# Kernel optimization log

Measured on AMD Instinct MI355X. Metric: run time of the kernel, lower is better.

## Reference

```python
import jax, jax.numpy as jnp
import numpy as np

D_MODEL = 1024
N_HEADS = 16
D_K = D_MODEL // N_HEADS
SEQ = 2048
BATCH = 2
THETA = 10000.0


def _rope(x, token_positions):
    # x: [b, h, s, dk]; token_positions: [s] int
    k = jnp.arange(0, D_K, 2, dtype=jnp.float32)
    freqs = 1.0 / (THETA ** (k / D_K))                    # [dk/2]
    angles = token_positions.astype(jnp.float32)[:, None] * freqs[None, :]  # [s, dk/2]
    cos = jnp.cos(angles)
    sin = jnp.sin(angles)
    x1 = x[..., 0::2]
    x2 = x[..., 1::2]
    r1 = x1 * cos - x2 * sin
    r2 = x1 * sin + x2 * cos
    out = jnp.stack([r1, r2], axis=-1)                    # [b,h,s,dk/2,2]
    return out.reshape(x.shape)


def setup_inputs() -> dict:
    key = jax.random.key(0)
    ks = jax.random.split(key, 5)
    sigma = np.sqrt(2.0 / (D_MODEL + D_MODEL))
    x = jax.random.normal(ks[0], (BATCH, SEQ, D_MODEL), dtype=jnp.float32)
    Wq = jax.random.truncated_normal(ks[1], -3.0, 3.0, (D_MODEL, D_MODEL), dtype=jnp.float32) * sigma
    Wk = jax.random.truncated_normal(ks[2], -3.0, 3.0, (D_MODEL, D_MODEL), dtype=jnp.float32) * sigma
    Wv = jax.random.truncated_normal(ks[3], -3.0, 3.0, (D_MODEL, D_MODEL), dtype=jnp.float32) * sigma
    Wo = jax.random.truncated_normal(ks[4], -3.0, 3.0, (D_MODEL, D_MODEL), dtype=jnp.float32) * sigma
    token_positions = jnp.arange(SEQ, dtype=jnp.int64)
    return {"x": x, "Wq": Wq, "Wk": Wk, "Wv": Wv, "Wo": Wo, "token_positions": token_positions}


def reference(x, Wq, Wk, Wv, Wo, token_positions):
    b, s, d = x.shape
    # projections: Linear stores weight [out,in], applies x @ W.T
    Q = x @ Wq.T
    K = x @ Wk.T
    V = x @ Wv.T
    # [b, s, h*dk] -> [b, h, s, dk]
    def split_heads(t):
        return t.reshape(b, s, N_HEADS, D_K).transpose(0, 2, 1, 3)
    Q, K, V = split_heads(Q), split_heads(K), split_heads(V)
    Q = _rope(Q, token_positions)
    K = _rope(K, token_positions)
    scale = 1.0 / np.sqrt(D_K).astype(np.float32)
    scores = jnp.einsum('bhqd,bhkd->bhqk', Q, K) * scale   # [b,h,s,s]
    causal = jnp.tril(jnp.ones((s, s), dtype=bool))
    scores = jnp.where(causal, scores, -jnp.inf)
    attn = jax.nn.softmax(scores, axis=-1)
    out = jnp.einsum('bhqk,bhkd->bhqd', attn, V)           # [b,h,s,dk]
    out = out.transpose(0, 2, 1, 3).reshape(b, s, d)
    return out @ Wo.T
```

## Files before the change

kernel.cpp:

```cpp
#include <hip/hip_runtime.h>
#include <hip/hip_bf16.h>
#include <stdint.h>

#define SEQL   2048
#define NBATCH 2
#define BSZ    4096
#define DMODEL 1024
#define NH     16
#define DK     64
#define NBH    32
#define NCHUNK_TOT 40

typedef __attribute__((ext_vector_type(8)))  short short8;
typedef __attribute__((ext_vector_type(4)))  short shortx4;
typedef __attribute__((ext_vector_type(4)))  float f32x4;
typedef __attribute__((ext_vector_type(16))) float f32x16;
typedef __attribute__((ext_vector_type(4)))  unsigned uint4v;
union PU { uint4v u; short8 s; };

__device__ __forceinline__ short f2b(float f) {
  unsigned u = __float_as_uint(f);
  u = (u + 0x7FFF + ((u >> 16) & 1)) >> 16;
  return (short)u;
}
__device__ __forceinline__ float b2f(short s) {
  return __uint_as_float(((unsigned)(unsigned short)s) << 16);
}
__device__ __forceinline__ unsigned cvtpk(float lo, float hi) {
  unsigned r;
  asm("v_cvt_pk_bf16_f32 %0, %1, %2" : "=v"(r) : "v"(lo), "v"(hi));
  return r;
}

__device__ __forceinline__ void g2l16(const void* g, void* l) {
  __builtin_amdgcn_global_load_lds(
      (__attribute__((address_space(1))) void*)(uintptr_t)g,
      (__attribute__((address_space(3))) void*)l, 16, 0, 0);
}

__device__ __forceinline__ f32x4 mfma16(short8 a, short8 b, f32x4 c) {
  return __builtin_amdgcn_mfma_f32_16x16x32_bf16(a, b, c, 0, 0, 0);
}
__device__ __forceinline__ f32x16 mfma32(short8 a, short8 b, f32x16 c) {
  return __builtin_amdgcn_mfma_f32_32x32x16_bf16(a, b, c, 0, 0, 0);
}

__global__ void cvt_all(const float* __restrict__ x,  const float* __restrict__ wq,
                        const float* __restrict__ wk, const float* __restrict__ wv,
                        const float* __restrict__ wo, short* __restrict__ xb,
                        short* __restrict__ wqkv, short* __restrict__ wob) {
  long idx = ((long)blockIdx.x * 256 + threadIdx.x) * 4;
  const float* s; short* d; long off;
  if (idx < 4194304L)      { s = x;  d = xb;             off = idx; }
  else if (idx < 5242880L) { s = wq; d = wqkv;           off = idx - 4194304L; }
  else if (idx < 6291456L) { s = wk; d = wqkv + 1048576; off = idx - 5242880L; }
  else if (idx < 7340032L) { s = wv; d = wqkv + 2097152; off = idx - 6291456L; }
  else                     { s = wo; d = wob;            off = idx - 7340032L; }
  float4 v = *(const float4*)(s + off);
  shortx4 r;
  r[0] = f2b(v.x); r[1] = f2b(v.y); r[2] = f2b(v.z); r[3] = f2b(v.w);
  *(shortx4*)(d + off) = r;
}

template<int CBF16>
__global__ __launch_bounds__(256, 2)
void gemm_bt(const short* __restrict__ A, const short* __restrict__ B,
             void* __restrict__ Cv, int M, int N, int K,
             long bStride, long cStride) {
  __shared__ short As[4096];
  __shared__ short Bs[4096];
  B += (long)blockIdx.y * bStride;
  int nbn = N >> 7;
  int bm = blockIdx.x / nbn, bn = blockIdx.x % nbn;
  int tid = threadIdx.x, w = tid >> 6, l = tid & 63;
  int wm = w >> 1, wn = w & 1;
  int lr = l & 15, lg = l >> 4;
  int brow = bm << 7, bcol = bn << 7;

  const f32x4 fz = {0.f, 0.f, 0.f, 0.f};
  f32x4 acc[4][4];
#pragma unroll
  for (int xi = 0; xi < 4; ++xi)
#pragma unroll
    for (int yi = 0; yi < 4; ++yi) acc[xi][yi] = fz;

  for (int k0 = 0; k0 < K; k0 += 32) {
#pragma unroll
    for (int i = 0; i < 2; ++i) {
      int c = w * 2 + i;
      int chunk = c * 64 + l;
      int row = chunk >> 2, ch = chunk & 3;
      int gch = ch ^ ((row >> 1) & 3);
      g2l16(A + (long)(brow + row) * K + k0 + gch * 8, &As[c * 512]);
      g2l16(B + (long)(bcol + row) * K + k0 + gch * 8, &Bs[c * 512]);
    }
    __syncthreads();

    short8 af[4], bf[4];
#pragma unroll
    for (int xi = 0; xi < 4; ++xi) {
      int ar = wm * 64 + xi * 16 + lr;
      af[xi] = *(const short8*)&As[ar * 32 + ((lg ^ ((ar >> 1) & 3)) << 3)];
      int br = wn * 64 + xi * 16 + lr;
      bf[xi] = *(const short8*)&Bs[br * 32 + ((lg ^ ((br >> 1) & 3)) << 3)];
    }
#pragma unroll
    for (int xi = 0; xi < 4; ++xi)
#pragma unroll
      for (int yi = 0; yi < 4; ++yi)
        acc[xi][yi] = mfma16(af[xi], bf[yi], acc[xi][yi]);
    __syncthreads();
  }

  if (CBF16) {
    short* C = (short*)Cv + (long)blockIdx.y * cStride;
#pragma unroll
    for (int xi = 0; xi < 4; ++xi)
#pragma unroll
      for (int yi = 0; yi < 4; ++yi)
#pragma unroll
        for (int r = 0; r < 4; ++r) {
          int row = brow + wm * 64 + xi * 16 + lg * 4 + r;
          int col = bcol + wn * 64 + yi * 16 + lr;
          C[(long)row * N + col] = f2b(acc[xi][yi][r]);
        }
  } else {
    float* C = (float*)Cv;
#pragma unroll
    for (int xi = 0; xi < 4; ++xi)
#pragma unroll
      for (int yi = 0; yi < 4; ++yi)
#pragma unroll
        for (int r = 0; r < 4; ++r) {
          int row = brow + wm * 64 + xi * 16 + lg * 4 + r;
          int col = bcol + wn * 64 + yi * 16 + lr;
          C[(long)row * N + col] = acc[xi][yi][r];
        }
  }
}

__global__ void rope_split(const short* __restrict__ qkv, const int* __restrict__ tok,
                           short* __restrict__ Qh, short* __restrict__ Kh) {
  int t = blockIdx.x * 256 + threadIdx.x;
  int qd = t & 15, h = (t >> 4) & 15, bs = t >> 8;
  int b = bs >> 11, s = bs & 2047;
  float pos = (float)tok[s];
  long srcoff = (long)bs * 1024 + h * 64 + qd * 4;
  shortx4 q4 = *(const shortx4*)(qkv + srcoff);
  shortx4 k4 = *(const shortx4*)(qkv + 4194304L + srcoff);
  shortx4 qo, ko;
#pragma unroll
  for (int p = 0; p < 2; ++p) {
    int i = qd * 2 + p;
    float freq = exp2f(-(float)i * (13.287712379549449f / 32.0f));
    float ang = pos * freq;
    float sn, cs;
    sincosf(ang, &sn, &cs);
    float x1 = b2f(q4[p * 2]), x2 = b2f(q4[p * 2 + 1]);
    qo[p * 2]     = f2b((x1 * cs - x2 * sn) * 0.125f);
    qo[p * 2 + 1] = f2b((x1 * sn + x2 * cs) * 0.125f);
    float y1 = b2f(k4[p * 2]), y2 = b2f(k4[p * 2 + 1]);
    ko[p * 2]     = f2b(y1 * cs - y2 * sn);
    ko[p * 2 + 1] = f2b(y1 * sn + y2 * cs);
  }
  long outoff = ((long)(b * 16 + h) * 2048 + s) * 64 + qd * 4;
  *(shortx4*)(Qh + outoff) = qo;
  *(shortx4*)(Kh + outoff) = ko;
}

__global__ void vtrans(const short* __restrict__ Vlin, short* __restrict__ Vt) {
  __shared__ short tile[64][72];
  int s0 = blockIdx.x * 64;
  int bh = blockIdx.y;
  int b = bh >> 4, h = bh & 15;
  int t = threadIdx.x;
  int r = t >> 2, c0 = (t & 3) * 16;
  const short* src = Vlin + ((long)(b * 2048 + s0 + r)) * 1024 + h * 64 + c0;
  *(short8*)&tile[r][c0]     = *(const short8*)src;
  *(short8*)&tile[r][c0 + 8] = *(const short8*)(src + 8);
  __syncthreads();
  int d = t >> 2, sc0 = (t & 3) * 16;
  short8 o0, o1;
#pragma unroll
  for (int j = 0; j < 8; ++j) { o0[j] = tile[sc0 + j][d]; o1[j] = tile[sc0 + 8 + j][d]; }
  short* dst = Vt + ((long)(bh * 64 + d)) * 2048 + s0 + sc0;
  *(short8*)dst       = o0;
  *(short8*)(dst + 8) = o1;
}

__global__ __launch_bounds__(256, 4)
void attn_fwd(const short* __restrict__ Qh, const short* __restrict__ Kh,
              const short* __restrict__ Vt, short* __restrict__ poO,
              float* __restrict__ pmb, float* __restrict__ plb) {
  __shared__ short Ks[2][4096];
  __shared__ short Vs[2][4096];
  int xr = 39 - blockIdx.x;
  int qi, c = xr, nc = 1;
  for (qi = 0; qi < 16; ++qi) { nc = (qi >> 2) + 1; if (c < nc) break; c -= nc; }
  int n = 2 * qi + 2;
  int t0 = (c * n) / nc, t1 = ((c + 1) * n) / nc;
  int q0b = qi << 7;
  int bh = blockIdx.y;
  int tid = threadIdx.x, w = tid >> 6, l = tid & 63;
  int ql = l & 31, hi = l >> 5;
  const short* Qb = Qh + (long)bh * (2048 * 64);
  const short* Kb = Kh + (long)bh * (2048 * 64);
  const short* Vb = Vt + (long)bh * (64 * 2048);
  int qw = q0b + 32 * w;
  int qg = qw + ql;
  int pid = bh * NCHUNK_TOT + xr;

  short8 qf[4];
#pragma unroll
  for (int kc = 0; kc < 4; ++kc)
    qf[kc] = *(const short8*)(Qb + (long)qg * 64 + kc * 16 + hi * 8);

  f32x16 o0, o1;
#pragma unroll
  for (int r = 0; r < 16; ++r) { o0[r] = 0.f; o1[r] = 0.f; }
  float m = -1e30f, lsum = 0.f;

#define STAGE(t_, bufi_) do {                                                   \
    int s0_ = (t_) << 6;                                                        \
    _Pragma("unroll")                                                           \
    for (int i_ = 0; i_ < 2; ++i_) {                                            \
      int c_ = w + 4 * i_;                                                      \
      int g_ = c_ >> 2, cc_ = c_ & 3;                                           \
      g2l16(Kb + ((long)(s0_ + g_ * 32 + ql)) * 64 + cc_ * 16 + hi * 8,         \
            &Ks[bufi_][c_ * 512]);                                              \
      g2l16(Vb + ((long)(g_ * 32 + ql)) * 2048 + s0_ + cc_ * 16 + hi * 8,       \
            &Vs[bufi_][c_ * 512]);                                              \
    }                                                                           \
  } while (0)

  STAGE(t0, 0);

  for (int t = t0; t < t1; ++t) {
    int cur = (t - t0) & 1;
    if (t + 1 < t1) {
      STAGE(t + 1, cur ^ 1);
      asm volatile("s_waitcnt vmcnt(4)" ::: "memory");
    } else {
      asm volatile("s_waitcnt vmcnt(0)" ::: "memory");
    }
    __builtin_amdgcn_s_barrier();
    int s0 = t << 6;
    if (s0 <= qw + 31) {
      f32x16 sT0, sT1;
#pragma unroll
      for (int r = 0; r < 16; ++r) { sT0[r] = 0.f; sT1[r] = 0.f; }
      __builtin_amdgcn_s_setprio(1);
#pragma unroll
      for (int kc = 0; kc < 4; ++kc) {
        short8 k0 = *(const short8*)&Ks[cur][(kc * 64 + l) * 8];
        short8 k1 = *(const short8*)&Ks[cur][((4 + kc) * 64 + l) * 8];
        sT0 = mfma32(k0, qf[kc], sT0);
        sT1 = mfma32(k1, qf[kc], sT1);
      }
      __builtin_amdgcn_s_setprio(0);
      if (s0 + 63 > qw) {
#pragma unroll
        for (int r = 0; r < 16; ++r) {
          int kvl = (r & 3) + 8 * (r >> 2) + 4 * hi;
          if (s0 + kvl > qg)      sT0[r] = -1e30f;
          if (s0 + 32 + kvl > qg) sT1[r] = -1e30f;
        }
      }
      float pmax = sT0[0];
#pragma unroll
      for (int r = 1; r < 16; ++r) pmax = fmaxf(pmax, sT0[r]);
#pragma unroll
      for (int r = 0; r < 16; ++r) pmax = fmaxf(pmax, sT1[r]);
      pmax = fmaxf(pmax, __shfl_xor(pmax, 32));
      if (__any(pmax > m + 8.0f)) {
        float mn = fmaxf(m, pmax);
        float sf = exp2f((m - mn) * 1.44269504f);
        m = mn;
        lsum *= sf;
#pragma unroll
        for (int r = 0; r < 16; ++r) {
          int row = (r & 3) + 8 * (r >> 2) + 4 * hi;
          float fo = __shfl(sf, row);
          o0[r] *= fo; o1[r] *= fo;
        }
      }
      float rs = 0.f;
#pragma unroll
      for (int r = 0; r < 16; ++r) {
        float p = exp2f((sT0[r] - m) * 1.44269504f);
        sT0[r] = p; rs += p;
      }
#pragma unroll
      for (int r = 0; r < 16; ++r) {
        float p = exp2f((sT1[r] - m) * 1.44269504f);
        sT1[r] = p; rs += p;
      }
      rs += __shfl_xor(rs, 32);
      lsum += rs;
      unsigned cA0[4], cB0[4], cA1[4], cB1[4];
#pragma unroll
      for (int g = 0; g < 4; ++g) {
        cA0[g] = cvtpk(sT0[4 * g], sT0[4 * g + 1]);
        cB0[g] = cvtpk(sT0[4 * g + 2], sT0[4 * g + 3]);
        cA1[g] = cvtpk(sT1[4 * g], sT1[4 * g + 1]);
        cB1[g] = cvtpk(sT1[4 * g + 2], sT1[4 * g + 3]);
      }
      short8 pa[4];
#define PAK(kc2_, A_, B_, dst_) do {                                            \
        unsigned sA = hi ? A_[2*(kc2_)]   : A_[2*(kc2_)+1];                     \
        unsigned sB = hi ? B_[2*(kc2_)]   : B_[2*(kc2_)+1];                     \
        unsigned rA = (unsigned)__shfl_xor((int)sA, 32);                        \
        unsigned rB = (unsigned)__shfl_xor((int)sB, 32);                        \
        unsigned kA = hi ? A_[2*(kc2_)+1] : A_[2*(kc2_)];                       \
        unsigned kB = hi ? B_[2*(kc2_)+1] : B_[2*(kc2_)];                       \
        PU pu; pu.u = (uint4v){ hi ? rA : kA, hi ? rB : kB,                     \
                                hi ? kA : rA, hi ? kB : rB };                   \
        dst_ = pu.s;                                                            \
      } while (0)
      PAK(0, cA0, cB0, pa[0]);
      PAK(1, cA0, cB0, pa[1]);
      PAK(0, cA1, cB1, pa[2]);
      PAK(1, cA1, cB1, pa[3]);
#undef PAK
      __builtin_amdgcn_s_setprio(1);
#pragma unroll
      for (int kc = 0; kc < 4; ++kc) {
        short8 v0 = *(const short8*)&Vs[cur][(kc * 64 + l) * 8];
        short8 v1 = *(const short8*)&Vs[cur][((4 + kc) * 64 + l) * 8];
        o0 = mfma32(pa[kc], v0, o0);
        o1 = mfma32(pa[kc], v1, o1);
      }
      __builtin_amdgcn_s_setprio(0);
    }
    asm volatile("s_waitcnt lgkmcnt(0)" ::: "memory");
    __builtin_amdgcn_s_barrier();
  }
#undef STAGE

  if (hi == 0) {
    pmb[pid * 128 + w * 32 + ql] = m;
    plb[pid * 128 + w * 32 + ql] = lsum;
  }
#pragma unroll
  for (int r = 0; r < 16; ++r) {
    int row = (r & 3) + 8 * (r >> 2) + 4 * hi;
    long basep = ((long)pid * 128 + w * 32 + row) * 64;
    poO[basep + ql]      = f2b(o0[r]);
    poO[basep + 32 + ql] = f2b(o1[r]);
  }
}

__global__ void attn_combine(const short* __restrict__ poO,
                             const float* __restrict__ pmb,
                             const float* __restrict__ plb,
                             short* __restrict__ Oh) {
  int x = blockIdx.x, bh = blockIdx.y;
  int qi = x >> 2, sub = x & 3;
  int t = threadIdx.x;
  int r = sub * 32 + (t >> 3);
  int d0 = (t & 7) * 8;
  int nc = (qi >> 2) + 1;
  int prefix = 0;
  for (int j = 0; j < qi; ++j) prefix += (j >> 2) + 1;
  int base = bh * NCHUNK_TOT + prefix;
  float M = -1e30f;
  for (int i = 0; i < nc; ++i)
    M = fmaxf(M, pmb[(base + i) * 128 + r]);
  float acc0 = 0, acc1 = 0, acc2 = 0, acc3 = 0, acc4 = 0, acc5 = 0, acc6 = 0, acc7 = 0;
  float den = 0.f;
  for (int i = 0; i < nc; ++i) {
    float wgt = exp2f((pmb[(base + i) * 128 + r] - M) * 1.44269504f);
    den += wgt * plb[(base + i) * 128 + r];
    short8 ov = *(const short8*)&poO[((long)(base + i) * 128 + r) * 64 + d0];
    acc0 += wgt * b2f(ov[0]); acc1 += wgt * b2f(ov[1]);
    acc2 += wgt * b2f(ov[2]); acc3 += wgt * b2f(ov[3]);
    acc4 += wgt * b2f(ov[4]); acc5 += wgt * b2f(ov[5]);
    acc6 += wgt * b2f(ov[6]); acc7 += wgt * b2f(ov[7]);
  }
  float inv = 1.0f / den;
  int b = bh >> 4, h = bh & 15;
  int s = qi * 128 + r;
  short8 out;
  out[0] = f2b(acc0 * inv); out[1] = f2b(acc1 * inv);
  out[2] = f2b(acc2 * inv); out[3] = f2b(acc3 * inv);
  out[4] = f2b(acc4 * inv); out[5] = f2b(acc5 * inv);
  out[6] = f2b(acc6 * inv); out[7] = f2b(acc7 * inv);
  *(short8*)&Oh[((long)(b * 2048 + s)) * 1024 + h * 64 + d0] = out;
}

extern "C" void kernel_launch(void* const* d_in, const int* in_sizes, int n_in,
                              void* d_out, int out_size, void* d_ws, size_t ws_size,
                              hipStream_t stream) {
  const float* x  = (const float*)d_in[0];
  const float* wq = (const float*)d_in[1];
  const float* wk = (const float*)d_in[2];
  const float* wv = (const float*)d_in[3];
  const float* wo = (const float*)d_in[4];
  const int* tok  = (const int*)d_in[5];

  short* wsp  = (short*)d_ws;
  short* xb   = wsp;
  short* wqkv = xb + 4194304;
  short* wob  = wqkv + 3145728;
  short* qkv  = wob + 1048576;
  short* qh   = qkv + 12582912;
  short* kh   = qh + 4194304;
  short* vt   = kh + 4194304;
  short* oh   = vt + 4194304;

  short* poO = qkv;
  float* pmb = (float*)xb;
  float* plb = pmb + NCHUNK_TOT * NBH * 128;

  (void)in_sizes; (void)n_in; (void)out_size; (void)ws_size;

  cvt_all<<<8192, 256, 0, stream>>>(x, wq, wk, wv, wo, xb, wqkv, wob);
  gemm_bt<1><<<dim3(256, 3), 256, 0, stream>>>(xb, wqkv, qkv, 4096, 1024, 1024,
                                               1048576L, 4194304L);
  rope_split<<<4096, 256, 0, stream>>>(qkv, tok, qh, kh);
  vtrans<<<dim3(32, 32), 256, 0, stream>>>(qkv + 8388608, vt);
  attn_fwd<<<dim3(NCHUNK_TOT, 32), 256, 0, stream>>>(qh, kh, vt, poO, pmb, plb);
  attn_combine<<<dim3(64, 32), 256, 0, stream>>>(poO, pmb, plb, oh);
  gemm_bt<0><<<dim3(256, 1), 256, 0, stream>>>(oh, wob, d_out, 4096, 1024, 1024,
                                               0L, 0L);
}
```

Baseline: 137.8 us.

## Triple-buffer attention KV loads, skip masked half-tiles, fold log2e into Q

```diff
diff --git a/kernel.cpp b/kernel.cpp
--- a/kernel.cpp
+++ b/kernel.cpp
@@ -31,6 +31,7 @@
   asm("v_cvt_pk_bf16_f32 %0, %1, %2" : "=v"(r) : "v"(lo), "v"(hi));
   return r;
 }
+#define PLSWAP(a_, b_) asm("v_permlane32_swap_b32 %0, %1" : "+v"(a_), "+v"(b_))
 
 __device__ __forceinline__ void g2l16(const void* g, void* l) {
   __builtin_amdgcn_global_load_lds(
@@ -156,9 +157,10 @@
     float ang = pos * freq;
     float sn, cs;
     sincosf(ang, &sn, &cs);
+    const float QS = 0.125f * 1.44269504f;
     float x1 = b2f(q4[p * 2]), x2 = b2f(q4[p * 2 + 1]);
-    qo[p * 2]     = f2b((x1 * cs - x2 * sn) * 0.125f);
-    qo[p * 2 + 1] = f2b((x1 * sn + x2 * cs) * 0.125f);
+    qo[p * 2]     = f2b((x1 * cs - x2 * sn) * QS);
+    qo[p * 2 + 1] = f2b((x1 * sn + x2 * cs) * QS);
     float y1 = b2f(k4[p * 2]), y2 = b2f(k4[p * 2 + 1]);
     ko[p * 2]     = f2b(y1 * cs - y2 * sn);
     ko[p * 2 + 1] = f2b(y1 * sn + y2 * cs);
@@ -188,19 +190,19 @@
   *(short8*)(dst + 8) = o1;
 }
 
-__global__ __launch_bounds__(256, 4)
+__global__ __launch_bounds__(256, 3)
 void attn_fwd(const short* __restrict__ Qh, const short* __restrict__ Kh,
               const short* __restrict__ Vt, short* __restrict__ poO,
               float* __restrict__ pmb, float* __restrict__ plb) {
-  __shared__ short Ks[2][4096];
-  __shared__ short Vs[2][4096];
-  int xr = 39 - blockIdx.x;
+  __shared__ short Ks[3][4096];
+  __shared__ short Vs[3][4096];
+  int bh = blockIdx.x;
+  int xr = 39 - blockIdx.y;
   int qi, c = xr, nc = 1;
   for (qi = 0; qi < 16; ++qi) { nc = (qi >> 2) + 1; if (c < nc) break; c -= nc; }
   int n = 2 * qi + 2;
   int t0 = (c * n) / nc, t1 = ((c + 1) * n) / nc;
   int q0b = qi << 7;
-  int bh = blockIdx.y;
   int tid = threadIdx.x, w = tid >> 6, l = tid & 63;
   int ql = l & 31, hi = l >> 5;
   const short* Qb = Qh + (long)bh * (2048 * 64);
@@ -234,11 +236,15 @@
   } while (0)
 
   STAGE(t0, 0);
+  if (t0 + 1 < t1) STAGE(t0 + 1, 1);
+  int cur = 0;
 
   for (int t = t0; t < t1; ++t) {
-    int cur = (t - t0) & 1;
-    if (t + 1 < t1) {
-      STAGE(t + 1, cur ^ 1);
+    if (t + 2 < t1) {
+      int nb = cur + 2; if (nb >= 3) nb -= 3;
+      STAGE(t + 2, nb);
+      asm volatile("s_waitcnt vmcnt(8)" ::: "memory");
+    } else if (t + 1 < t1) {
       asm volatile("s_waitcnt vmcnt(4)" ::: "memory");
     } else {
       asm volatile("s_waitcnt vmcnt(0)" ::: "memory");
@@ -246,6 +252,7 @@
     __builtin_amdgcn_s_barrier();
     int s0 = t << 6;
     if (s0 <= qw + 31) {
+      bool upper = (s0 + 32 <= qw + 31);
       f32x16 sT0, sT1;
 #pragma unroll
       for (int r = 0; r < 16; ++r) { sT0[r] = 0.f; sT1[r] = 0.f; }
@@ -253,28 +260,41 @@
 #pragma unroll
       for (int kc = 0; kc < 4; ++kc) {
         short8 k0 = *(const short8*)&Ks[cur][(kc * 64 + l) * 8];
-        short8 k1 = *(const short8*)&Ks[cur][((4 + kc) * 64 + l) * 8];
         sT0 = mfma32(k0, qf[kc], sT0);
-        sT1 = mfma32(k1, qf[kc], sT1);
+      }
+      if (upper) {
+#pragma unroll
+        for (int kc = 0; kc < 4; ++kc) {
+          short8 k1 = *(const short8*)&Ks[cur][((4 + kc) * 64 + l) * 8];
+          sT1 = mfma32(k1, qf[kc], sT1);
+        }
       }
       __builtin_amdgcn_s_setprio(0);
       if (s0 + 63 > qw) {
 #pragma unroll
         for (int r = 0; r < 16; ++r) {
           int kvl = (r & 3) + 8 * (r >> 2) + 4 * hi;
-          if (s0 + kvl > qg)      sT0[r] = -1e30f;
-          if (s0 + 32 + kvl > qg) sT1[r] = -1e30f;
+          if (s0 + kvl > qg) sT0[r] = -1e30f;
+        }
+        if (upper) {
+#pragma unroll
+          for (int r = 0; r < 16; ++r) {
+            int kvl = (r & 3) + 8 * (r >> 2) + 4 * hi;
+            if (s0 + 32 + kvl > qg) sT1[r] = -1e30f;
+          }
         }
       }
       float pmax = sT0[0];
 #pragma unroll
       for (int r = 1; r < 16; ++r) pmax = fmaxf(pmax, sT0[r]);
-#pragma unroll
-      for (int r = 0; r < 16; ++r) pmax = fmaxf(pmax, sT1[r]);
+      if (upper) {
+#pragma unroll
+        for (int r = 0; r < 16; ++r) pmax = fmaxf(pmax, sT1[r]);
+      }
       pmax = fmaxf(pmax, __shfl_xor(pmax, 32));
-      if (__any(pmax > m + 8.0f)) {
+      if (__any(pmax > m + 11.5416f)) {
         float mn = fmaxf(m, pmax);
-        float sf = exp2f((m - mn) * 1.44269504f);
+        float sf = exp2f(m - mn);
         m = mn;
         lsum *= sf;
 #pragma unroll
@@ -287,53 +307,65 @@
       float rs = 0.f;
 #pragma unroll
       for (int r = 0; r < 16; ++r) {
-        float p = exp2f((sT0[r] - m) * 1.44269504f);
+        float p = exp2f(sT0[r] - m);
         sT0[r] = p; rs += p;
       }
-#pragma unroll
-      for (int r = 0; r < 16; ++r) {
-        float p = exp2f((sT1[r] - m) * 1.44269504f);
-        sT1[r] = p; rs += p;
+      if (upper) {
+#pragma unroll
+        for (int r = 0; r < 16; ++r) {
+          float p = exp2f(sT1[r] - m);
+          sT1[r] = p; rs += p;
+        }
       }
       rs += __shfl_xor(rs, 32);
       lsum += rs;
-      unsigned cA0[4], cB0[4], cA1[4], cB1[4];
-#pragma unroll
-      for (int g = 0; g < 4; ++g) {
-        cA0[g] = cvtpk(sT0[4 * g], sT0[4 * g + 1]);
-        cB0[g] = cvtpk(sT0[4 * g + 2], sT0[4 * g + 3]);
-        cA1[g] = cvtpk(sT1[4 * g], sT1[4 * g + 1]);
-        cB1[g] = cvtpk(sT1[4 * g + 2], sT1[4 * g + 3]);
-      }
       short8 pa[4];
-#define PAK(kc2_, A_, B_, dst_) do {                                            \
-        unsigned sA = hi ? A_[2*(kc2_)]   : A_[2*(kc2_)+1];                     \
-        unsigned sB = hi ? B_[2*(kc2_)]   : B_[2*(kc2_)+1];                     \
-        unsigned rA = (unsigned)__shfl_xor((int)sA, 32);                        \
-        unsigned rB = (unsigned)__shfl_xor((int)sB, 32);                        \
-        unsigned kA = hi ? A_[2*(kc2_)+1] : A_[2*(kc2_)];                       \
-        unsigned kB = hi ? B_[2*(kc2_)+1] : B_[2*(kc2_)];                       \
-        PU pu; pu.u = (uint4v){ hi ? rA : kA, hi ? rB : kB,                     \
-                                hi ? kA : rA, hi ? kB : rB };                   \
-        dst_ = pu.s;                                                            \
-      } while (0)
-      PAK(0, cA0, cB0, pa[0]);
-      PAK(1, cA0, cB0, pa[1]);
-      PAK(0, cA1, cB1, pa[2]);
-      PAK(1, cA1, cB1, pa[3]);
-#undef PAK
+      {
+        unsigned cA[4], cB[4];
+#pragma unroll
+        for (int g = 0; g < 4; ++g) {
+          cA[g] = cvtpk(sT0[4 * g], sT0[4 * g + 1]);
+          cB[g] = cvtpk(sT0[4 * g + 2], sT0[4 * g + 3]);
+        }
+        PLSWAP(cA[0], cA[1]); PLSWAP(cB[0], cB[1]);
+        PLSWAP(cA[2], cA[3]); PLSWAP(cB[2], cB[3]);
+        PU p0; p0.u = (uint4v){cA[0], cB[0], cA[1], cB[1]}; pa[0] = p0.s;
+        PU p1; p1.u = (uint4v){cA[2], cB[2], cA[3], cB[3]}; pa[1] = p1.s;
+      }
+      if (upper) {
+        unsigned cA[4], cB[4];
+#pragma unroll
+        for (int g = 0; g < 4; ++g) {
+          cA[g] = cvtpk(sT1[4 * g], sT1[4 * g + 1]);
+          cB[g] = cvtpk(sT1[4 * g + 2], sT1[4 * g + 3]);
+        }
+        PLSWAP(cA[0], cA[1]); PLSWAP(cB[0], cB[1]);
+        PLSWAP(cA[2], cA[3]); PLSWAP(cB[2], cB[3]);
+        PU p2; p2.u = (uint4v){cA[0], cB[0], cA[1], cB[1]}; pa[2] = p2.s;
+        PU p3; p3.u = (uint4v){cA[2], cB[2], cA[3], cB[3]}; pa[3] = p3.s;
+      }
       __builtin_amdgcn_s_setprio(1);
 #pragma unroll
-      for (int kc = 0; kc < 4; ++kc) {
+      for (int kc = 0; kc < 2; ++kc) {
         short8 v0 = *(const short8*)&Vs[cur][(kc * 64 + l) * 8];
         short8 v1 = *(const short8*)&Vs[cur][((4 + kc) * 64 + l) * 8];
         o0 = mfma32(pa[kc], v0, o0);
         o1 = mfma32(pa[kc], v1, o1);
       }
+      if (upper) {
+#pragma unroll
+        for (int kc = 2; kc < 4; ++kc) {
+          short8 v0 = *(const short8*)&Vs[cur][(kc * 64 + l) * 8];
+          short8 v1 = *(const short8*)&Vs[cur][((4 + kc) * 64 + l) * 8];
+          o0 = mfma32(pa[kc], v0, o0);
+          o1 = mfma32(pa[kc], v1, o1);
+        }
+      }
       __builtin_amdgcn_s_setprio(0);
     }
     asm volatile("s_waitcnt lgkmcnt(0)" ::: "memory");
     __builtin_amdgcn_s_barrier();
+    ++cur; if (cur >= 3) cur -= 3;
   }
 #undef STAGE
 
@@ -369,7 +401,7 @@
   float acc0 = 0, acc1 = 0, acc2 = 0, acc3 = 0, acc4 = 0, acc5 = 0, acc6 = 0, acc7 = 0;
   float den = 0.f;
   for (int i = 0; i < nc; ++i) {
-    float wgt = exp2f((pmb[(base + i) * 128 + r] - M) * 1.44269504f);
+    float wgt = exp2f(pmb[(base + i) * 128 + r] - M);
     den += wgt * plb[(base + i) * 128 + r];
     short8 ov = *(const short8*)&poO[((long)(base + i) * 128 + r) * 64 + d0];
     acc0 += wgt * b2f(ov[0]); acc1 += wgt * b2f(ov[1]);
@@ -419,7 +451,7 @@
                                                1048576L, 4194304L);
   rope_split<<<4096, 256, 0, stream>>>(qkv, tok, qh, kh);
   vtrans<<<dim3(32, 32), 256, 0, stream>>>(qkv + 8388608, vt);
-  attn_fwd<<<dim3(NCHUNK_TOT, 32), 256, 0, stream>>>(qh, kh, vt, poO, pmb, plb);
+  attn_fwd<<<dim3(32, NCHUNK_TOT), 256, 0, stream>>>(qh, kh, vt, poO, pmb, plb);
   attn_combine<<<dim3(64, 32), 256, 0, stream>>>(poO, pmb, plb, oh);
   gemm_bt<0><<<dim3(256, 1), 256, 0, stream>>>(oh, wob, d_out, 4096, 1024, 1024,
                                                0L, 0L);
```

New measurement: 130.5 us. -5.3%, faster.
